# Kernel optimization log

Measured on AMD Instinct MI355X. Metric: run time of the kernel, lower is better.

The kernel has to match this reference:

```python
import jax, jax.numpy as jnp
import numpy as np

N_CELLS = 50000
N_GENES = 2000
HIDDEN = 128
HEADS = 4
HEAD_DIM = HIDDEN // HEADS
E_FULL = 800000
E_PRUNED = 400000
LN_EPS = 1e-6
NEG_SLOPE = 0.2


def setup_inputs() -> dict:
    key = jax.random.key(0)
    ks = jax.random.split(key, 20)
    s_in = 1.0 / np.sqrt(N_GENES)
    s_h = 1.0 / np.sqrt(HIDDEN)
    inp = {
        "node_features": jax.random.normal(ks[0], (N_CELLS, N_GENES), jnp.float32),
        "full_edge_index": jax.random.randint(ks[1], (2, E_FULL), 0, N_CELLS, jnp.int64 if jax.config.jax_enable_x64 else jnp.int32),
        "full_edge_weights": jax.random.uniform(ks[2], (E_FULL, 1), jnp.float32),
        "pruned_edge_index": jax.random.randint(ks[3], (2, E_PRUNED), 0, N_CELLS, jnp.int64 if jax.config.jax_enable_x64 else jnp.int32),
        "pruned_edge_weights": jax.random.uniform(ks[4], (E_PRUNED, 1), jnp.float32),
        "alpha": jax.random.uniform(ks[5], (), jnp.float32),
        # input projection
        "ip_w": jax.random.normal(ks[6], (N_GENES, HIDDEN), jnp.float32) * s_in,
        "ip_b": jnp.zeros((HIDDEN,), jnp.float32),
        # GAT full graph
        "gf_wsrc": jax.random.normal(ks[7], (HIDDEN, HIDDEN), jnp.float32) * s_h,
        "gf_wdst": jax.random.normal(ks[8], (HIDDEN, HIDDEN), jnp.float32) * s_h,
        "gf_wedge": jax.random.normal(ks[9], (1, HIDDEN), jnp.float32),
        "gf_attn": jax.random.normal(ks[10], (HEADS, HEAD_DIM), jnp.float32) * (1.0 / np.sqrt(HEAD_DIM)),
        "gf_bias": jnp.zeros((HIDDEN,), jnp.float32),
        # GAT pruned graph
        "gp_wsrc": jax.random.normal(ks[11], (HIDDEN, HIDDEN), jnp.float32) * s_h,
        "gp_wdst": jax.random.normal(ks[12], (HIDDEN, HIDDEN), jnp.float32) * s_h,
        "gp_wedge": jax.random.normal(ks[13], (1, HIDDEN), jnp.float32),
        "gp_attn": jax.random.normal(ks[14], (HEADS, HEAD_DIM), jnp.float32) * (1.0 / np.sqrt(HEAD_DIM)),
        "gp_bias": jnp.zeros((HIDDEN,), jnp.float32),
        # LayerNorm
        "ln_scale": jnp.ones((HIDDEN,), jnp.float32),
        "ln_bias": jnp.zeros((HIDDEN,), jnp.float32),
    }
    return inp


def _gatv2(h, edge_index, edge_w, wsrc, wdst, wedge, attn, bias):
    """GATv2 with edge features: e_ij = a_h . leaky_relu(Ws h_i + Wd h_j + We w_ij),
    segment-softmax over destination nodes, scatter-aggregate Ws h_src, concat heads."""
    n = h.shape[0]
    src, dst = edge_index[0], edge_index[1]
    hs = (h @ wsrc).reshape(n, HEADS, HEAD_DIM)
    hd = (h @ wdst).reshape(n, HEADS, HEAD_DIM)
    ew = (edge_w @ wedge).reshape(-1, HEADS, HEAD_DIM)  # [E,H,D]
    z = jax.nn.leaky_relu(hs[src] + hd[dst] + ew, NEG_SLOPE)  # [E,H,D]
    logits = jnp.einsum('ehd,hd->eh', z, attn)  # [E,H]
    # segment softmax over incoming edges of each dst node
    m = jax.ops.segment_max(logits, dst, num_segments=n)
    m = jnp.where(jnp.isfinite(m), m, 0.0)
    ex = jnp.exp(logits - m[dst])
    denom = jax.ops.segment_sum(ex, dst, num_segments=n)
    att = ex / (denom[dst] + 1e-16)  # [E,H]
    out = jax.ops.segment_sum(att[..., None] * hs[src], dst, num_segments=n)  # [n,H,D]
    return out.reshape(n, HIDDEN) + bias


def _layer_norm(x, scale, bias):
    mu = jnp.mean(x, axis=-1, keepdims=True)
    var = jnp.mean(jnp.square(x - mu), axis=-1, keepdims=True)
    return (x - mu) * jax.lax.rsqrt(var + LN_EPS) * scale + bias


def reference(node_features, full_edge_index, full_edge_weights, pruned_edge_index,
              pruned_edge_weights, alpha, ip_w, ip_b,
              gf_wsrc, gf_wdst, gf_wedge, gf_attn, gf_bias,
              gp_wsrc, gp_wdst, gp_wedge, gp_attn, gp_bias,
              ln_scale, ln_bias):
    h = node_features @ ip_w + ip_b  # [n, hidden]
    h_full = _gatv2(h, full_edge_index, full_edge_weights, gf_wsrc, gf_wdst, gf_wedge, gf_attn, gf_bias)
    h_pruned = _gatv2(h, pruned_edge_index, pruned_edge_weights, gp_wsrc, gp_wdst, gp_wedge, gp_attn, gp_bias)
    h = (1.0 - alpha) * h_full + alpha * h_pruned
    h = jax.nn.elu(h)
    return _layer_norm(h, ln_scale, ln_bias)
```

## Files before the change

### kernel.cpp

```cpp
#include <hip/hip_runtime.h>
#include <hip/hip_bf16.h>

#define N_GENES 2000
#define SA 72
#define SH 136

typedef __attribute__((ext_vector_type(8))) short frag8;
typedef __attribute__((ext_vector_type(4))) float facc4;

static __device__ __forceinline__ unsigned short f2bf(float f) {
    unsigned int u = __float_as_uint(f);
    unsigned int r = (u + 0x7FFFu + ((u >> 16) & 1u)) >> 16;
    return (unsigned short)r;
}
static __device__ __forceinline__ ushort2 pk2(float a, float b) {
    __hip_bfloat162 r = __float22bfloat162_rn(float2{a, b});
    return *(ushort2*)&r;
}

__global__ void prep_deg(const float* __restrict__ ip_w,
                         const float* __restrict__ ws_f, const float* __restrict__ wd_f,
                         const float* __restrict__ ws_p, const float* __restrict__ wd_p,
                         unsigned short* __restrict__ Bt1,
                         unsigned short* __restrict__ Bf, unsigned short* __restrict__ Bp,
                         const int* __restrict__ dst_f, int Ef,
                         const int* __restrict__ dst_p, int Ep,
                         int* __restrict__ deg, int N) {
    int idx = blockIdx.x * blockDim.x + threadIdx.x;
    if (idx < 128 * 2048) {
        int nrow = idx >> 11, k = idx & 2047;
        unsigned short v = 0;
        if (k < N_GENES) v = f2bf(ip_w[(size_t)k * 128 + nrow]);
        Bt1[idx] = v;
    } else if (idx < 128 * 2048 + 2 * 256 * 128) {
        int q = idx - 128 * 2048;
        int g = q >> 15;
        int r = (q >> 7) & 255;
        int k = q & 127;
        const float* w = (g == 0) ? (r < 128 ? ws_f : wd_f) : (r < 128 ? ws_p : wd_p);
        (g == 0 ? Bf : Bp)[(r << 7) | k] = f2bf(w[k * 128 + (r & 127)]);
    } else {
        int e = idx - (128 * 2048 + 2 * 256 * 128);
        if (e < Ef) atomicAdd(&deg[dst_f[e]], 1);
        else if (e < Ef + Ep) atomicAdd(&deg[N + dst_p[e - Ef]], 1);
    }
}

__global__ __launch_bounds__(256) void seg_assign(const int* __restrict__ deg,
                                                  int* __restrict__ offs,
                                                  int* __restrict__ cur,
                                                  unsigned int* __restrict__ counter, int n2) {
    __shared__ int wbase[4];
    int t = threadIdx.x;
    int i = blockIdx.x * 256 + t;
    int lane = t & 63, wv = t >> 6;
    int c = (i < n2) ? deg[i] : 0;
    int incl = c;
#pragma unroll
    for (int o = 1; o < 64; o <<= 1) {
        int y = __shfl_up(incl, o);
        if (lane >= o) incl += y;
    }
    if (lane == 63) wbase[wv] = incl;
    __syncthreads();
    if (t == 0) {
        int s0 = wbase[0], s1 = wbase[1], s2 = wbase[2], s3 = wbase[3];
        int b = (int)atomicAdd(counter, (unsigned int)(s0 + s1 + s2 + s3));
        wbase[0] = b;
        wbase[1] = b + s0;
        wbase[2] = b + s0 + s1;
        wbase[3] = b + s0 + s1 + s2;
    }
    __syncthreads();
    int start = wbase[wv] + incl - c;
    if (i < n2) { offs[i] = start; cur[i] = start; }
}

__global__ __launch_bounds__(256) void gemm_fill(const float* __restrict__ A,
                                                 const unsigned short* __restrict__ Bt,
                                                 const float* __restrict__ bias,
                                                 const unsigned short* __restrict__ Bf,
                                                 const unsigned short* __restrict__ Bp,
                                                 unsigned short* __restrict__ Cf,
                                                 unsigned short* __restrict__ Cp,
                                                 int M, int K, int gemmBlocks,
                                                 const int* __restrict__ src_f,
                                                 const int* __restrict__ dst_f,
                                                 const float* __restrict__ ew_f, int Ef,
                                                 const int* __restrict__ src_p,
                                                 const int* __restrict__ dst_p,
                                                 const float* __restrict__ ew_p, int Ep,
                                                 int* __restrict__ cur,
                                                 int2* __restrict__ srcw, int N) {
    if (blockIdx.x >= gemmBlocks) {
        int e = (blockIdx.x - gemmBlocks) * 256 + threadIdx.x;
        if (e >= Ef + Ep) return;
        int g = (e >= Ef);
        int ee = g ? e - Ef : e;
        int d = g ? dst_p[ee] : dst_f[ee];
        int node = g ? N + d : d;
        int p = atomicAdd(&cur[node], 1);
        int s = g ? src_p[ee] : src_f[ee];
        float w = g ? ew_p[ee] : ew_f[ee];
        srcw[p] = make_int2(s, __float_as_int(w));
        return;
    }
    const int Kpad = 2048;
    __shared__ __align__(16) unsigned short lA[64 * SA];
    __shared__ __align__(16) unsigned short lH[64 * SH];
    int t = threadIdx.x, lane = t & 63, wv = t >> 6;
    int lr = lane & 15, lq = lane >> 4;
    facc4 acc[4][2];
#pragma unroll
    for (int i = 0; i < 4; i++)
#pragma unroll
        for (int j = 0; j < 2; j++) acc[i][j] = (facc4){0.f, 0.f, 0.f, 0.f};
    int row_base = blockIdx.x * 64;

    int ar_r[4], ar_c[4];
    const float* ar_p[4];
#pragma unroll
    for (int j = 0; j < 4; j++) {
        int q = j * 256 + t;
        ar_r[j] = q >> 4;
        ar_c[j] = (q & 15) * 4;
        int rg = row_base + ar_r[j];
        if (rg >= M) rg = M - 1;
        ar_p[j] = A + (size_t)rg * K + ar_c[j];
    }
    const unsigned short* bp[4];
#pragma unroll
    for (int ks = 0; ks < 2; ks++)
#pragma unroll
        for (int ni = 0; ni < 2; ni++) {
            int col = wv * 32 + ni * 16 + lr;
            bp[ks * 2 + ni] = Bt + (size_t)col * Kpad + ks * 32 + lq * 8;
        }

    float4 ar[4];
    frag8 bfr[4];
#pragma unroll
    for (int j = 0; j < 4; j++) ar[j] = *(const float4*)(ar_p[j]);
#pragma unroll
    for (int f = 0; f < 4; f++) bfr[f] = *(const frag8*)(bp[f]);

    for (int k0 = 0; k0 < Kpad; k0 += 64) {
        __syncthreads();
#pragma unroll
        for (int j = 0; j < 4; j++) {
            ushort2 u01 = pk2(ar[j].x, ar[j].y);
            ushort2 u23 = pk2(ar[j].z, ar[j].w);
            ushort4 u = {u01.x, u01.y, u23.x, u23.y};
            *(ushort4*)&lA[ar_r[j] * SA + ar_c[j]] = u;
        }
        __syncthreads();
        int kn = k0 + 64;
        frag8 bfn[4];
        if (kn < Kpad) {
#pragma unroll
            for (int j = 0; j < 4; j++) {
                int kk = kn + ar_c[j];
                float4 v = {0.f, 0.f, 0.f, 0.f};
                if (kk < K) v = *(const float4*)(ar_p[j] + kn);
                ar[j] = v;
            }
#pragma unroll
            for (int f = 0; f < 4; f++) bfn[f] = *(const frag8*)(bp[f] + kn);
        }
#pragma unroll
        for (int ks = 0; ks < 2; ks++) {
            frag8 af[4];
#pragma unroll
            for (int mi = 0; mi < 4; mi++)
                af[mi] = *(const frag8*)&lA[(mi * 16 + lr) * SA + ks * 32 + lq * 8];
#pragma unroll
            for (int mi = 0; mi < 4; mi++)
#pragma unroll
                for (int ni = 0; ni < 2; ni++)
                    acc[mi][ni] = __builtin_amdgcn_mfma_f32_16x16x32_bf16(af[mi], bfr[ks * 2 + ni], acc[mi][ni], 0, 0, 0);
        }
        if (kn < Kpad) {
#pragma unroll
            for (int f = 0; f < 4; f++) bfr[f] = bfn[f];
        }
    }
    __syncthreads();
#pragma unroll
    for (int mi = 0; mi < 4; mi++) {
#pragma unroll
        for (int r = 0; r < 4; r++) {
            int row = mi * 16 + lq * 4 + r;
#pragma unroll
            for (int ni = 0; ni < 2; ni++) {
                int col = wv * 32 + ni * 16 + lr;
                lH[row * SH + col] = f2bf(acc[mi][ni][r] + bias[col]);
            }
        }
    }
    __syncthreads();
#pragma unroll 1
    for (int g = 0; g < 2; g++) {
        const unsigned short* B2 = g ? Bp : Bf;
        unsigned short* Cb = g ? Cp : Cf;
        facc4 a2[4][4];
#pragma unroll
        for (int i = 0; i < 4; i++)
#pragma unroll
            for (int j = 0; j < 4; j++) a2[i][j] = (facc4){0.f, 0.f, 0.f, 0.f};
#pragma unroll
        for (int ks = 0; ks < 4; ks++) {
            frag8 af[4], bf[4];
#pragma unroll
            for (int mi = 0; mi < 4; mi++)
                af[mi] = *(const frag8*)&lH[(mi * 16 + lr) * SH + ks * 32 + lq * 8];
#pragma unroll
            for (int ni = 0; ni < 4; ni++)
                bf[ni] = *(const frag8*)(B2 + ((wv * 64 + ni * 16 + lr) << 7) + ks * 32 + lq * 8);
#pragma unroll
            for (int mi = 0; mi < 4; mi++)
#pragma unroll
                for (int ni = 0; ni < 4; ni++)
                    a2[mi][ni] = __builtin_amdgcn_mfma_f32_16x16x32_bf16(af[mi], bf[ni], a2[mi][ni], 0, 0, 0);
        }
#pragma unroll
        for (int mi = 0; mi < 4; mi++) {
#pragma unroll
            for (int r = 0; r < 4; r++) {
                int row = row_base + mi * 16 + lq * 4 + r;
                if (row < M) {
#pragma unroll
                    for (int ni = 0; ni < 4; ni++) {
                        int col = wv * 64 + ni * 16 + lr;
                        Cb[(size_t)row * 256 + col] = f2bf(a2[mi][ni][r]);
                    }
                }
            }
        }
    }
}

__global__ __launch_bounds__(256) void gat2(const int* __restrict__ offs,
                                            const int* __restrict__ deg,
                                            const int2* __restrict__ srcw,
                                            const unsigned short* __restrict__ hshd_f,
                                            const unsigned short* __restrict__ hshd_p,
                                            const float* __restrict__ wedge_f,
                                            const float* __restrict__ attn_f,
                                            const float* __restrict__ bias_f,
                                            const float* __restrict__ wedge_p,
                                            const float* __restrict__ attn_p,
                                            const float* __restrict__ bias_p,
                                            float* __restrict__ out_full,
                                            float* __restrict__ out_pruned, int N) {
    int wid = blockIdx.x * 4 + (threadIdx.x >> 6);
    if (wid * 2 >= 2 * N) return;
    int lane = threadIdx.x & 63;
    int half = lane >> 5;
    int wl = lane & 31;
    int node = wid * 2 + half;
    int g = node >= N;
    int onode = g ? node - N : node;
    const unsigned short* hshd = g ? hshd_p : hshd_f;
    const float* wedge = g ? wedge_p : wedge_f;
    const float* attn = g ? attn_p : attn_f;
    const float* bias = g ? bias_p : bias_f;
    float* out = g ? out_pruned : out_full;
    int d4 = wl * 4;
    const float LOG2E = 1.4426950408889634f;
    float4 wv4 = *(const float4*)&wedge[d4];
    float4 av4 = *(const float4*)&attn[d4];
    av4.x *= LOG2E; av4.y *= LOG2E; av4.z *= LOG2E; av4.w *= LOG2E;
    uint2 hdr = *(const uint2*)&hshd[(size_t)onode * 256 + 128 + d4];
    const float hd0 = __uint_as_float(hdr.x << 16);
    const float hd1 = __uint_as_float(hdr.x & 0xffff0000u);
    const float hd2 = __uint_as_float(hdr.y << 16);
    const float hd3 = __uint_as_float(hdr.y & 0xffff0000u);
    int s = offs[node], cnt = deg[node];
    if (cnt <= 0) s = 0;
    int mc = max(cnt, __shfl_xor(cnt, 32));
    float m = -INFINITY, l = 0.f;
    float a0 = 0.f, a1 = 0.f, a2 = 0.f, a3 = 0.f;
    if (mc > 0) {
        int last = s + (cnt > 0 ? cnt : 1) - 1;
        auto CL = [last](int j) { return j > last ? last : j; };
        int2 e0 = srcw[CL(s)], e1 = srcw[CL(s + 1)], e2 = srcw[CL(s + 2)], e3 = srcw[CL(s + 3)];
        int2 e4 = srcw[CL(s + 4)], e5 = srcw[CL(s + 5)];
        uint2 hr0 = *(const uint2*)&hshd[(size_t)e0.x * 256 + d4];
        uint2 hr1 = *(const uint2*)&hshd[(size_t)e1.x * 256 + d4];
        uint2 hr2 = *(const uint2*)&hshd[(size_t)e2.x * 256 + d4];
        uint2 hr3 = *(const uint2*)&hshd[(size_t)e3.x * 256 + d4];
        for (int i = 0; i < mc; i += 2) {
            int2 ea = srcw[CL(s + i + 6)], eb = srcw[CL(s + i + 7)];
            uint2 hr4 = *(const uint2*)&hshd[(size_t)e4.x * 256 + d4];
            uint2 hr5 = *(const uint2*)&hshd[(size_t)e5.x * 256 + d4];
            {
                float h0 = __uint_as_float(hr0.x << 16);
                float h1 = __uint_as_float(hr0.x & 0xffff0000u);
                float h2 = __uint_as_float(hr0.y << 16);
                float h3 = __uint_as_float(hr0.y & 0xffff0000u);
                float w = __int_as_float(e0.y);
                float z0 = fmaf(w, wv4.x, h0 + hd0); z0 = (z0 > 0.f) ? z0 : 0.2f * z0;
                float z1 = fmaf(w, wv4.y, h1 + hd1); z1 = (z1 > 0.f) ? z1 : 0.2f * z1;
                float z2 = fmaf(w, wv4.z, h2 + hd2); z2 = (z2 > 0.f) ? z2 : 0.2f * z2;
                float z3 = fmaf(w, wv4.w, h3 + hd3); z3 = (z3 > 0.f) ? z3 : 0.2f * z3;
                float t = fmaf(z3, av4.w, fmaf(z2, av4.z, fmaf(z1, av4.y, z0 * av4.x)));
                t += __shfl_xor(t, 1);
                t += __shfl_xor(t, 2);
                t += __shfl_xor(t, 4);
                float mn = fmaxf(m, t);
                float sc = __builtin_amdgcn_exp2f(m - mn);
                float p = __builtin_amdgcn_exp2f(t - mn);
                p = (i < cnt) ? p : 0.f;
                l = l * sc + p;
                a0 = fmaf(p, h0, a0 * sc);
                a1 = fmaf(p, h1, a1 * sc);
                a2 = fmaf(p, h2, a2 * sc);
                a3 = fmaf(p, h3, a3 * sc);
                m = mn;
            }
            {
                float h0 = __uint_as_float(hr1.x << 16);
                float h1 = __uint_as_float(hr1.x & 0xffff0000u);
                float h2 = __uint_as_float(hr1.y << 16);
                float h3 = __uint_as_float(hr1.y & 0xffff0000u);
                float w = __int_as_float(e1.y);
                float z0 = fmaf(w, wv4.x, h0 + hd0); z0 = (z0 > 0.f) ? z0 : 0.2f * z0;
                float z1 = fmaf(w, wv4.y, h1 + hd1); z1 = (z1 > 0.f) ? z1 : 0.2f * z1;
                float z2 = fmaf(w, wv4.z, h2 + hd2); z2 = (z2 > 0.f) ? z2 : 0.2f * z2;
                float z3 = fmaf(w, wv4.w, h3 + hd3); z3 = (z3 > 0.f) ? z3 : 0.2f * z3;
                float t = fmaf(z3, av4.w, fmaf(z2, av4.z, fmaf(z1, av4.y, z0 * av4.x)));
                t += __shfl_xor(t, 1);
                t += __shfl_xor(t, 2);
                t += __shfl_xor(t, 4);
                float mn = fmaxf(m, t);
                float sc = __builtin_amdgcn_exp2f(m - mn);
                float p = __builtin_amdgcn_exp2f(t - mn);
                p = (i + 1 < cnt) ? p : 0.f;
                l = l * sc + p;
                a0 = fmaf(p, h0, a0 * sc);
                a1 = fmaf(p, h1, a1 * sc);
                a2 = fmaf(p, h2, a2 * sc);
                a3 = fmaf(p, h3, a3 * sc);
                m = mn;
            }
            e0 = e2; e1 = e3; e2 = e4; e3 = e5; e4 = ea; e5 = eb;
            hr0 = hr2; hr1 = hr3; hr2 = hr4; hr3 = hr5;
        }
    }
    float inv = 1.f / (l + 1e-16f);
    const float4 bv = *(const float4*)&bias[d4];
    float4 o;
    o.x = fmaf(a0, inv, bv.x);
    o.y = fmaf(a1, inv, bv.y);
    o.z = fmaf(a2, inv, bv.z);
    o.w = fmaf(a3, inv, bv.w);
    *(float4*)&out[(size_t)onode * 128 + d4] = o;
}

__global__ __launch_bounds__(256) void final_kernel(const float* __restrict__ hf,
                                                    float* __restrict__ out,
                                                    const float* __restrict__ alpha_p,
                                                    const float* __restrict__ scale,
                                                    const float* __restrict__ beta, int n) {
    int node = blockIdx.x * 4 + (threadIdx.x >> 6);
    if (node >= n) return;
    int lane = threadIdx.x & 63;
    int d2 = lane * 2;
    float a = *alpha_p;
    float2 f = *(const float2*)&hf[(size_t)node * 128 + d2];
    float2 p = *(const float2*)&out[(size_t)node * 128 + d2];
    float x0 = (1.f - a) * f.x + a * p.x;
    float x1 = (1.f - a) * f.y + a * p.y;
    x0 = (x0 > 0.f) ? x0 : expm1f(x0);
    x1 = (x1 > 0.f) ? x1 : expm1f(x1);
    float sm = x0 + x1;
#pragma unroll
    for (int o = 32; o >= 1; o >>= 1) sm += __shfl_xor(sm, o);
    float mu = sm * (1.f / 128.f);
    float d0 = x0 - mu, d1 = x1 - mu;
    float v = d0 * d0 + d1 * d1;
#pragma unroll
    for (int o = 32; o >= 1; o >>= 1) v += __shfl_xor(v, o);
    float rstd = rsqrtf(v * (1.f / 128.f) + 1e-6f);
    const float2 sv = *(const float2*)&scale[d2];
    const float2 bv = *(const float2*)&beta[d2];
    float2 o2;
    o2.x = d0 * rstd * sv.x + bv.x;
    o2.y = d1 * rstd * sv.y + bv.y;
    *(float2*)&out[(size_t)node * 128 + d2] = o2;
}

extern "C" void kernel_launch(void* const* d_in, const int* in_sizes, int n_in,
                              void* d_out, int out_size, void* d_ws, size_t ws_size,
                              hipStream_t stream) {
    const float* nf = (const float*)d_in[0];
    const int* fei = (const int*)d_in[1];
    const float* few = (const float*)d_in[2];
    const int* pei = (const int*)d_in[3];
    const float* pew = (const float*)d_in[4];
    const float* alpha = (const float*)d_in[5];
    const float* ip_w = (const float*)d_in[6];
    const float* ip_b = (const float*)d_in[7];
    const float* gf_wsrc = (const float*)d_in[8];
    const float* gf_wdst = (const float*)d_in[9];
    const float* gf_wedge = (const float*)d_in[10];
    const float* gf_attn = (const float*)d_in[11];
    const float* gf_bias = (const float*)d_in[12];
    const float* gp_wsrc = (const float*)d_in[13];
    const float* gp_wdst = (const float*)d_in[14];
    const float* gp_wedge = (const float*)d_in[15];
    const float* gp_attn = (const float*)d_in[16];
    const float* gp_bias = (const float*)d_in[17];
    const float* ln_scale = (const float*)d_in[18];
    const float* ln_bias = (const float*)d_in[19];

    const int N = in_sizes[0] / N_GENES;
    const int Ef = in_sizes[1] / 2;
    const int Ep = in_sizes[3] / 2;
    const int Etot = Ef + Ep;
    const int n2 = 2 * N;

    char* base = (char*)d_ws;
    size_t off = 0;
    auto carve = [&](size_t bytes) -> char* {
        char* p = base + off;
        off = (off + bytes + 255) & ~(size_t)255;
        return p;
    };
    unsigned short* Bt1 = (unsigned short*)carve((size_t)128 * 2048 * 2);
    unsigned short* Bf = (unsigned short*)carve(256 * 128 * 2);
    unsigned short* Bp = (unsigned short*)carve(256 * 128 * 2);
    unsigned short* hshd_f = (unsigned short*)carve((size_t)N * 256 * 2);
    unsigned short* hshd_p = (unsigned short*)carve((size_t)N * 256 * 2);
    float* h_full = (float*)carve((size_t)N * 128 * 4);
    unsigned int* counter = (unsigned int*)carve(4);
    int* deg = (int*)carve((size_t)n2 * 4);
    int* offs = (int*)carve((size_t)n2 * 4);
    int* cur = (int*)carve((size_t)n2 * 4);
    int2* srcw = (int2*)carve((size_t)Etot * 8);
    float* out_f = (float*)d_out;

    const int* src_f = fei;
    const int* dst_f = fei + Ef;
    const int* src_p = pei;
    const int* dst_p = pei + Ep;

    hipMemsetAsync(counter, 0, 256 + (size_t)n2 * 4, stream);

    int prepWork = 128 * 2048 + 2 * 256 * 128;
    prep_deg<<<(prepWork + Etot + 255) / 256, 256, 0, stream>>>(
        ip_w, gf_wsrc, gf_wdst, gp_wsrc, gp_wdst, Bt1, Bf, Bp,
        dst_f, Ef, dst_p, Ep, deg, N);

    seg_assign<<<(n2 + 255) / 256, 256, 0, stream>>>(deg, offs, cur, counter, n2);

    int gb1 = (N + 63) / 64;
    int fillb = (Etot + 255) / 256;
    gemm_fill<<<gb1 + fillb, 256, 0, stream>>>(nf, Bt1, ip_b, Bf, Bp, hshd_f, hshd_p,
                                               N, N_GENES, gb1,
                                               src_f, dst_f, few, Ef,
                                               src_p, dst_p, pew, Ep,
                                               cur, srcw, N);

    int gwaves = (n2 + 1) / 2;
    gat2<<<(gwaves + 3) / 4, 256, 0, stream>>>(offs, deg, srcw, hshd_f, hshd_p,
                                               gf_wedge, gf_attn, gf_bias,
                                               gp_wedge, gp_attn, gp_bias,
                                               h_full, out_f, N);

    final_kernel<<<(N + 3) / 4, 256, 0, stream>>>(h_full, out_f, alpha, ln_scale, ln_bias, N);
    (void)ws_size; (void)n_in; (void)out_size;
}
```

Baseline: 783.1 us.

## Fuse both GAT aggregations with blend, ELU and LayerNorm into one kernel

Each half-wave now processes one node through both the full and pruned GAT streams in sequence, then blends, applies ELU and LayerNorm in registers and writes the final output. This removes the h_full intermediate buffer, the round trip of both GAT outputs through global memory, and a separate kernel launch. In exchange each wave does the two edge loops serially, so parallelism per node pair is halved and there is less latency hiding across the two graphs.

```diff
diff --git a/kernel.cpp b/kernel.cpp
--- a/kernel.cpp
+++ b/kernel.cpp
@@ -239,33 +239,12 @@
     }
 }
 
-__global__ __launch_bounds__(256) void gat2(const int* __restrict__ offs,
-                                            const int* __restrict__ deg,
-                                            const int2* __restrict__ srcw,
-                                            const unsigned short* __restrict__ hshd_f,
-                                            const unsigned short* __restrict__ hshd_p,
-                                            const float* __restrict__ wedge_f,
-                                            const float* __restrict__ attn_f,
-                                            const float* __restrict__ bias_f,
-                                            const float* __restrict__ wedge_p,
-                                            const float* __restrict__ attn_p,
-                                            const float* __restrict__ bias_p,
-                                            float* __restrict__ out_full,
-                                            float* __restrict__ out_pruned, int N) {
-    int wid = blockIdx.x * 4 + (threadIdx.x >> 6);
-    if (wid * 2 >= 2 * N) return;
-    int lane = threadIdx.x & 63;
-    int half = lane >> 5;
-    int wl = lane & 31;
-    int node = wid * 2 + half;
-    int g = node >= N;
-    int onode = g ? node - N : node;
-    const unsigned short* hshd = g ? hshd_p : hshd_f;
-    const float* wedge = g ? wedge_p : wedge_f;
-    const float* attn = g ? attn_p : attn_f;
-    const float* bias = g ? bias_p : bias_f;
-    float* out = g ? out_pruned : out_full;
-    int d4 = wl * 4;
+static __device__ __forceinline__ float4 gat_stream(const unsigned short* __restrict__ hshd,
+                                                    const float* __restrict__ wedge,
+                                                    const float* __restrict__ attn,
+                                                    const float* __restrict__ bias,
+                                                    const int2* __restrict__ srcw,
+                                                    int s, int cnt, int onode, int d4) {
     const float LOG2E = 1.4426950408889634f;
     float4 wv4 = *(const float4*)&wedge[d4];
     float4 av4 = *(const float4*)&attn[d4];
@@ -275,7 +254,6 @@
     const float hd1 = __uint_as_float(hdr.x & 0xffff0000u);
     const float hd2 = __uint_as_float(hdr.y << 16);
     const float hd3 = __uint_as_float(hdr.y & 0xffff0000u);
-    int s = offs[node], cnt = deg[node];
     if (cnt <= 0) s = 0;
     int mc = max(cnt, __shfl_xor(cnt, 32));
     float m = -INFINITY, l = 0.f;
@@ -354,40 +332,65 @@
     o.y = fmaf(a1, inv, bv.y);
     o.z = fmaf(a2, inv, bv.z);
     o.w = fmaf(a3, inv, bv.w);
-    *(float4*)&out[(size_t)onode * 128 + d4] = o;
-}
-
-__global__ __launch_bounds__(256) void final_kernel(const float* __restrict__ hf,
-                                                    float* __restrict__ out,
-                                                    const float* __restrict__ alpha_p,
-                                                    const float* __restrict__ scale,
-                                                    const float* __restrict__ beta, int n) {
-    int node = blockIdx.x * 4 + (threadIdx.x >> 6);
-    if (node >= n) return;
+    return o;
+}
+
+__global__ __launch_bounds__(256) void gat_final(const int* __restrict__ offs,
+                                                 const int* __restrict__ deg,
+                                                 const int2* __restrict__ srcw,
+                                                 const unsigned short* __restrict__ hshd_f,
+                                                 const unsigned short* __restrict__ hshd_p,
+                                                 const float* __restrict__ wedge_f,
+                                                 const float* __restrict__ attn_f,
+                                                 const float* __restrict__ bias_f,
+                                                 const float* __restrict__ wedge_p,
+                                                 const float* __restrict__ attn_p,
+                                                 const float* __restrict__ bias_p,
+                                                 const float* __restrict__ alpha_p,
+                                                 const float* __restrict__ scale,
+                                                 const float* __restrict__ beta,
+                                                 float* __restrict__ out, int N) {
+    int wid = blockIdx.x * 4 + (threadIdx.x >> 6);
+    if (wid * 2 >= N) return;
     int lane = threadIdx.x & 63;
-    int d2 = lane * 2;
+    int half = lane >> 5;
+    int wl = lane & 31;
+    int node = wid * 2 + half;
+    bool valid = node < N;
+    int nc = valid ? node : N - 1;
+    int d4 = wl * 4;
+    int sF = offs[nc], cF = valid ? deg[nc] : 0;
+    float4 f = gat_stream(hshd_f, wedge_f, attn_f, bias_f, srcw, sF, cF, nc, d4);
+    int sP = offs[N + nc], cP = valid ? deg[N + nc] : 0;
+    float4 p = gat_stream(hshd_p, wedge_p, attn_p, bias_p, srcw, sP, cP, nc, d4);
     float a = *alpha_p;
-    float2 f = *(const float2*)&hf[(size_t)node * 128 + d2];
-    float2 p = *(const float2*)&out[(size_t)node * 128 + d2];
     float x0 = (1.f - a) * f.x + a * p.x;
     float x1 = (1.f - a) * f.y + a * p.y;
+    float x2 = (1.f - a) * f.z + a * p.z;
+    float x3 = (1.f - a) * f.w + a * p.w;
     x0 = (x0 > 0.f) ? x0 : expm1f(x0);
     x1 = (x1 > 0.f) ? x1 : expm1f(x1);
-    float sm = x0 + x1;
-#pragma unroll
-    for (int o = 32; o >= 1; o >>= 1) sm += __shfl_xor(sm, o);
+    x2 = (x2 > 0.f) ? x2 : expm1f(x2);
+    x3 = (x3 > 0.f) ? x3 : expm1f(x3);
+    float sm = x0 + x1 + x2 + x3;
+#pragma unroll
+    for (int o = 16; o >= 1; o >>= 1) sm += __shfl_xor(sm, o);
     float mu = sm * (1.f / 128.f);
-    float d0 = x0 - mu, d1 = x1 - mu;
-    float v = d0 * d0 + d1 * d1;
-#pragma unroll
-    for (int o = 32; o >= 1; o >>= 1) v += __shfl_xor(v, o);
+    float d0 = x0 - mu, d1 = x1 - mu, d2 = x2 - mu, d3 = x3 - mu;
+    float v = d0 * d0 + d1 * d1 + d2 * d2 + d3 * d3;
+#pragma unroll
+    for (int o = 16; o >= 1; o >>= 1) v += __shfl_xor(v, o);
     float rstd = rsqrtf(v * (1.f / 128.f) + 1e-6f);
-    const float2 sv = *(const float2*)&scale[d2];
-    const float2 bv = *(const float2*)&beta[d2];
-    float2 o2;
-    o2.x = d0 * rstd * sv.x + bv.x;
-    o2.y = d1 * rstd * sv.y + bv.y;
-    *(float2*)&out[(size_t)node * 128 + d2] = o2;
+    const float4 sv = *(const float4*)&scale[d4];
+    const float4 bv = *(const float4*)&beta[d4];
+    if (valid) {
+        float4 o4;
+        o4.x = fmaf(d0 * rstd, sv.x, bv.x);
+        o4.y = fmaf(d1 * rstd, sv.y, bv.y);
+        o4.z = fmaf(d2 * rstd, sv.z, bv.z);
+        o4.w = fmaf(d3 * rstd, sv.w, bv.w);
+        *(float4*)&out[(size_t)node * 128 + d4] = o4;
+    }
 }
 
 extern "C" void kernel_launch(void* const* d_in, const int* in_sizes, int n_in,
@@ -432,7 +435,6 @@
     unsigned short* Bp = (unsigned short*)carve(256 * 128 * 2);
     unsigned short* hshd_f = (unsigned short*)carve((size_t)N * 256 * 2);
     unsigned short* hshd_p = (unsigned short*)carve((size_t)N * 256 * 2);
-    float* h_full = (float*)carve((size_t)N * 128 * 4);
     unsigned int* counter = (unsigned int*)carve(4);
     int* deg = (int*)carve((size_t)n2 * 4);
     int* offs = (int*)carve((size_t)n2 * 4);
@@ -462,12 +464,10 @@
                                                src_p, dst_p, pew, Ep,
                                                cur, srcw, N);
 
-    int gwaves = (n2 + 1) / 2;
-    gat2<<<(gwaves + 3) / 4, 256, 0, stream>>>(offs, deg, srcw, hshd_f, hshd_p,
-                                               gf_wedge, gf_attn, gf_bias,
-                                               gp_wedge, gp_attn, gp_bias,
-                                               h_full, out_f, N);
-
-    final_kernel<<<(N + 3) / 4, 256, 0, stream>>>(h_full, out_f, alpha, ln_scale, ln_bias, N);
+    int gwaves = (N + 1) / 2;
+    gat_final<<<(gwaves + 3) / 4, 256, 0, stream>>>(offs, deg, srcw, hshd_f, hshd_p,
+                                                    gf_wedge, gf_attn, gf_bias,
+                                                    gp_wedge, gp_attn, gp_bias,
+                                                    alpha, ln_scale, ln_bias, out_f, N);
     (void)ws_size; (void)n_in; (void)out_size;
 }
```

After: 781.2 us. Within noise of the previous version (-0.2%).
